# Kernel optimization log

Measured on AMD Instinct MI355X. Metric: run time of the kernel, lower is better.

Reference implementation:

```python
import jax, jax.numpy as jnp
import numpy as np

TOPK = 8            # args.topk
SWAP_RATIO = 0.3    # args.swap_ratio
NUM_SPECIAL = 999   # first non-special wordpiece id in bert-base-uncased


def setup_inputs() -> dict:
    key = jax.random.key(0)
    k0, k1, k2, k3, k4, k5 = jax.random.split(key, 6)
    B, S, V, D = 4, 512, 30522, 768
    return {
        "delta_grad": jax.random.normal(k0, (B, S, D), jnp.float32),
        "src_embeds": jax.random.normal(k1, (B, S, D), jnp.float32),
        "embedding_matrix": jax.random.normal(k2, (V, D), jnp.float32),
        "src_tokens": jax.random.randint(k3, (B, S), 0, V),
        "pred_lm": jax.random.normal(k4, (B, S, V), jnp.float32),
        "attention_mask": jnp.ones((B, S), jnp.int32),
        "rand_u": jax.random.uniform(k5, (B, S), jnp.float32),
    }


def reference(delta_grad, src_embeds, embedding_matrix, src_tokens, pred_lm, attention_mask, rand_u):
    B, S, D = delta_grad.shape
    V = embedding_matrix.shape[0]
    neg_inf = jnp.float32(-np.inf)

    # dir_dot_grad = -(prev_dot - new_dot) = new_dot - prev_dot
    new_dot = jnp.einsum('bsd,vd->bsv', delta_grad, embedding_matrix)   # [B,S,V]
    prev_dot = jnp.einsum('bsd,bsd->bs', delta_grad, src_embeds)        # [B,S]
    dir_dot_grad = new_dot - prev_dot[..., None]

    # pairwise euclidean distance between src_embeds and vocab embeddings
    src_sq = jnp.sum(src_embeds * src_embeds, axis=-1)                  # [B,S]
    vocab_sq = jnp.sum(embedding_matrix * embedding_matrix, axis=-1)    # [V]
    dot = jnp.einsum('bsd,vd->bsv', src_embeds, embedding_matrix)       # [B,S,V]
    sq_norm = src_sq[..., None] + vocab_sq[None, None, :] - 2.0 * dot
    dir_norm = jnp.sqrt(jax.nn.relu(sq_norm) + 1e-20)

    dir_dot_grad = dir_dot_grad / dir_norm

    # LM top-k allowed-token mask (scatter of 0 into a -inf mask in torch)
    _, topk_idx = jax.lax.top_k(pred_lm, TOPK)                          # [B,S,K]
    topk_idx = topk_idx * attention_mask[..., None].astype(topk_idx.dtype)
    bi = jnp.arange(B)[:, None, None]
    si = jnp.arange(S)[None, :, None]
    allowed = jnp.zeros((B, S, V), bool).at[bi, si, topk_idx].set(True)

    filtered = jnp.where(allowed, dir_dot_grad, neg_inf)
    # special tokens [:999] -> -inf (overrides any topk scatter there)
    filtered = jnp.where(jnp.arange(V)[None, None, :] < NUM_SPECIAL, neg_inf, filtered)
    # forbid keeping the original token
    filtered = jnp.where(jnp.arange(V)[None, None, :] == src_tokens[..., None], neg_inf, filtered)

    adv_flip = jnp.argmax(filtered, axis=2)                             # [B,S]

    # swap mask: non-special positions, Bernoulli(swap_ratio)
    no_special = src_tokens >= NUM_SPECIAL
    swap = rand_u > (1.0 - SWAP_RATIO)
    mask_idx = (no_special & swap).astype(src_tokens.dtype)

    adv_tokens = src_tokens * (1 - mask_idx) + adv_flip.astype(src_tokens.dtype) * mask_idx
    return adv_tokens
```

## Files before the change

### kernel.cpp

```cpp
#include <hip/hip_runtime.h>
#include <math.h>

constexpr int TOPK = 8;
constexpr int NUM_SPECIAL = 999;
constexpr int V = 30522;
constexpr int D = 768;
constexpr int BLOCK = 256;
constexpr int V2 = V / 2;
constexpr int NQ = 14;
constexpr int NK = (V2 + BLOCK - 1) / BLOCK;
constexpr int CAP = 512;
constexpr int HOTCAP = 64;

__device__ __forceinline__ unsigned long long fkey(float v, unsigned int idx) {
    unsigned int u = __float_as_uint(v);
    u = ((int)u < 0) ? ~u : (u | 0x80000000u);
    return ((unsigned long long)u << 32) | (unsigned long long)(~idx);
}

__device__ __forceinline__ void net8(float (&L)[TOPK], float t) {
    #pragma unroll
    for (int j = 0; j < TOPK; ++j) {
        float m = fmaxf(L[j], t); t = fminf(L[j], t); L[j] = m;
    }
}

__device__ __forceinline__ void cmpx(float& a, float& b) {
    float m = fmaxf(a, b), n = fminf(a, b); a = m; b = n;
}
__device__ __forceinline__ void bitonic_sort8_desc(float (&v)[TOPK]) {
    cmpx(v[0], v[4]); cmpx(v[1], v[5]); cmpx(v[2], v[6]); cmpx(v[3], v[7]);
    cmpx(v[0], v[2]); cmpx(v[1], v[3]); cmpx(v[4], v[6]); cmpx(v[5], v[7]);
    cmpx(v[0], v[1]); cmpx(v[2], v[3]); cmpx(v[4], v[5]); cmpx(v[6], v[7]);
}

__device__ __forceinline__ void wave_extract8(float (&cur)[TOPK], int lane,
                                              float* dst) {
    #pragma unroll
    for (int r = 0; r < TOPK; ++r) {
        float m = cur[0];
        int ml = lane;
        #pragma unroll
        for (int off = 1; off < 64; off <<= 1) {
            float om = __shfl_xor(m, off, 64);
            int   ol = __shfl_xor(ml, off, 64);
            if (om > m || (om == m && ol < ml)) { m = om; ml = ol; }
        }
        if (lane == ml) {
            #pragma unroll
            for (int j = 0; j < TOPK - 1; ++j) cur[j] = cur[j + 1];
            cur[TOPK - 1] = -INFINITY;
        }
        if (lane == 0) dst[r] = m;
    }
}

__global__ __launch_bounds__(BLOCK, 8) void dvat_kernel(
    const float* __restrict__ delta_grad,
    const float* __restrict__ src_embeds,
    const float* __restrict__ emb,
    const int*   __restrict__ src_tokens,
    const float* __restrict__ pred_lm,
    const int*   __restrict__ attn,
    const float* __restrict__ rand_u,
    int* __restrict__ out)
{
    const int pos = blockIdx.x;
    const int tid = threadIdx.x;
    const int lane = tid & 63;
    const int wave = tid >> 6;

    __shared__ float  sm32[32];
    __shared__ float  s_g8;
    __shared__ int    s_hot[HOTCAP];
    __shared__ int    s_nhot;
    __shared__ int    s_ncand;
    __shared__ unsigned long long sh_cand64[CAP];
    __shared__ int    s_cand[TOPK];
    __shared__ double s_scores[TOPK];
    __shared__ double s_pd[4], s_ssq[4];
    __shared__ float  shf[2 * D];

    if (tid == 0) { s_nhot = 0; s_ncand = 0; }

    const float2* row2 = (const float2*)(pred_lm + (size_t)pos * V);

    float vx[TOPK], vy[TOPK];
    #pragma unroll
    for (int j = 0; j < TOPK; ++j) { vx[j] = -INFINITY; vy[j] = -INFINITY; }

    int i = tid;
    for (int q = 0; q < NQ; ++q, i += 4 * BLOCK) {
        float2 a = row2[i];
        float2 b = row2[i + BLOCK];
        float2 c = row2[i + 2 * BLOCK];
        float2 d = row2[i + 3 * BLOCK];
        net8(vx, a.x); net8(vy, a.y);
        net8(vx, b.x); net8(vy, b.y);
        net8(vx, c.x); net8(vy, c.y);
        net8(vx, d.x); net8(vy, d.y);
    }
    for (; i < V2; i += BLOCK) {
        float2 f = row2[i];
        net8(vx, f.x); net8(vy, f.y);
    }

    float v8[TOPK];
    #pragma unroll
    for (int j = 0; j < TOPK; ++j) v8[j] = fmaxf(vx[j], vy[TOPK - 1 - j]);
    bitonic_sort8_desc(v8);
    const float tmax = v8[0];

    wave_extract8(v8, lane, &sm32[wave * 8]);
    __syncthreads();

    if (wave == 0) {
        float c = (lane < 32) ? sm32[lane] : -INFINITY;
        float m = -INFINITY;
        #pragma unroll
        for (int r = 0; r < TOPK; ++r) {
            m = c; int ml = lane;
            #pragma unroll
            for (int off = 1; off < 64; off <<= 1) {
                float om = __shfl_xor(m, off, 64);
                int   ol = __shfl_xor(ml, off, 64);
                if (om > m || (om == m && ol < ml)) { m = om; ml = ol; }
            }
            if (lane == ml) c = -INFINITY;
        }
        if (lane == 0) s_g8 = m;
    }
    __syncthreads();
    const float g8 = s_g8;

    if (tmax >= g8) {
        int p = atomicAdd(&s_nhot, 1);
        if (p < HOTCAP) s_hot[p] = tid;
    }
    __syncthreads();

    if (s_nhot <= HOTCAP) {
        const int nhot = s_nhot;
        const int total = nhot * NK;
        for (int w = tid; w < total; w += BLOCK) {
            const int h = w / NK;
            const int k = w - h * NK;
            const int i2 = s_hot[h] + (k << 8);
            if (i2 < V2) {
                float2 f = row2[i2];
                if (f.x >= g8) {
                    int p = atomicAdd(&s_ncand, 1);
                    if (p < CAP) sh_cand64[p] = fkey(f.x, (unsigned)(2 * i2));
                }
                if (f.y >= g8) {
                    int p = atomicAdd(&s_ncand, 1);
                    if (p < CAP) sh_cand64[p] = fkey(f.y, (unsigned)(2 * i2 + 1));
                }
            }
        }
    } else {
        for (int i2 = tid; i2 < V2; i2 += BLOCK) {
            float2 f = row2[i2];
            if (f.x >= g8) {
                int p = atomicAdd(&s_ncand, 1);
                if (p < CAP) sh_cand64[p] = fkey(f.x, (unsigned)(2 * i2));
            }
            if (f.y >= g8) {
                int p = atomicAdd(&s_ncand, 1);
                if (p < CAP) sh_cand64[p] = fkey(f.y, (unsigned)(2 * i2 + 1));
            }
        }
    }
    __syncthreads();
    const int ncand = min(s_ncand, CAP);

    for (int it = 0; it < TOPK; ++it) {
        if (tid < 64) {
            unsigned long long m = 0ull; int ms = 0;
            for (int j = tid; j < ncand; j += 64) {
                unsigned long long x = sh_cand64[j];
                if (x > m) { m = x; ms = j; }
            }
            #pragma unroll
            for (int off = 32; off; off >>= 1) {
                unsigned long long om = __shfl_down(m, off, 64);
                int os = __shfl_down(ms, off, 64);
                if (om > m) { m = om; ms = os; }
            }
            if (tid == 0) {
                s_cand[it] = (m == 0ull) ? 0 : (int)(~(unsigned int)m);
                sh_cand64[ms] = 0ull;
            }
        }
        __syncthreads();
    }

    if (tid == 0 && attn[pos] == 0) {
        #pragma unroll
        for (int k = 0; k < TOPK; ++k) s_cand[k] = 0;
    }
    __syncthreads();

    const float* dg = delta_grad + (size_t)pos * D;
    const float* se = src_embeds + (size_t)pos * D;

    double pd = 0.0, ssq = 0.0;
    for (int ii = tid; ii < D; ii += BLOCK) {
        float g = dg[ii], e = se[ii];
        shf[ii] = g;
        shf[D + ii] = e;
        pd  += (double)g * (double)e;
        ssq += (double)e * (double)e;
    }
    #pragma unroll
    for (int off = 32; off; off >>= 1) {
        pd  += __shfl_down(pd, off, 64);
        ssq += __shfl_down(ssq, off, 64);
    }
    if (lane == 0) { s_pd[wave] = pd; s_ssq[wave] = ssq; }
    __syncthreads();

    const double prev_dot = s_pd[0] + s_pd[1] + s_pd[2] + s_pd[3];
    const double src_sq   = s_ssq[0] + s_ssq[1] + s_ssq[2] + s_ssq[3];

    #pragma unroll
    for (int kk = 0; kk < 2; ++kk) {
        const int k = 2 * wave + kk;
        const int v = s_cand[k];
        const float* ev = emb + (size_t)v * D;
        double ddg = 0.0, dse = 0.0, dvv = 0.0;
        for (int ii = lane; ii < D; ii += 64) {
            double e = (double)ev[ii];
            ddg += e * (double)shf[ii];
            dse += e * (double)shf[D + ii];
            dvv += e * e;
        }
        #pragma unroll
        for (int off = 32; off; off >>= 1) {
            ddg += __shfl_down(ddg, off, 64);
            dse += __shfl_down(dse, off, 64);
            dvv += __shfl_down(dvv, off, 64);
        }
        if (lane == 0) {
            double sq = src_sq + dvv - 2.0 * dse;
            if (sq < 0.0) sq = 0.0;
            double dn = sqrt(sq + 1e-20);
            s_scores[k] = (ddg - prev_dot) / dn;
        }
    }
    __syncthreads();

    if (tid == 0) {
        const int src_tok = src_tokens[pos];
        int best = 0;
        double best_s = 0.0;
        bool found = false;
        #pragma unroll
        for (int k = 0; k < TOPK; ++k) {
            const int v = s_cand[k];
            if (v < NUM_SPECIAL || v == src_tok) continue;
            const double sc = s_scores[k];
            if (!found || sc > best_s || (sc == best_s && v < best)) {
                best = v; best_s = sc; found = true;
            }
        }
        const int adv_flip = found ? best : 0;
        const bool no_special = (src_tok >= NUM_SPECIAL);
        const bool swap = (rand_u[pos] > 0.7f);
        out[pos] = (no_special && swap) ? adv_flip : src_tok;
    }
}

extern "C" void kernel_launch(void* const* d_in, const int* in_sizes, int n_in,
                              void* d_out, int out_size, void* d_ws, size_t ws_size,
                              hipStream_t stream) {
    const float* delta_grad = (const float*)d_in[0];
    const float* src_embeds = (const float*)d_in[1];
    const float* emb        = (const float*)d_in[2];
    const int*   src_tokens = (const int*)d_in[3];
    const float* pred_lm    = (const float*)d_in[4];
    const int*   attn       = (const int*)d_in[5];
    const float* randu      = (const float*)d_in[6];
    int* out = (int*)d_out;

    const int BS = in_sizes[3];
    dvat_kernel<<<BS, BLOCK, 0, stream>>>(delta_grad, src_embeds, emb,
                                          src_tokens, pred_lm, attn, randu, out);
}
```

Measured before the change: 414.0 us.

## Use aligned float4 loads with sorted-merge top-8 and hoist per-position dot products

The row scan of pred_lm now uses 16-byte float4 loads aligned by handling a two-element head or tail per row. Each group of 8 values is sorted with a network and merged into the running top-8, which replaces 8 serial insertions. The delta_grad/src_embeds load and reductions move to the start of the kernel, which removes one barrier and overlaps that load with the scan. It adds special-case handling of the edge elements, which is a correctness risk if the alignment arithmetic is wrong.

```diff
diff --git a/kernel.cpp b/kernel.cpp
--- a/kernel.cpp
+++ b/kernel.cpp
@@ -6,9 +6,8 @@
 constexpr int V = 30522;
 constexpr int D = 768;
 constexpr int BLOCK = 256;
-constexpr int V2 = V / 2;
-constexpr int NQ = 14;
-constexpr int NK = (V2 + BLOCK - 1) / BLOCK;
+constexpr int NF4 = 7630;
+constexpr int NK4 = 30;
 constexpr int CAP = 512;
 constexpr int HOTCAP = 64;
 
@@ -18,20 +17,35 @@
     return ((unsigned long long)u << 32) | (unsigned long long)(~idx);
 }
 
+__device__ __forceinline__ void cmpx(float& a, float& b) {
+    float m = fmaxf(a, b), n = fminf(a, b); a = m; b = n;
+}
+
+__device__ __forceinline__ void sort8_desc(float (&c)[8]) {
+    cmpx(c[0],c[1]); cmpx(c[2],c[3]); cmpx(c[4],c[5]); cmpx(c[6],c[7]);
+    cmpx(c[0],c[2]); cmpx(c[1],c[3]); cmpx(c[1],c[2]);
+    cmpx(c[4],c[6]); cmpx(c[5],c[7]); cmpx(c[5],c[6]);
+    cmpx(c[0],c[4]); cmpx(c[1],c[5]); cmpx(c[2],c[6]); cmpx(c[3],c[7]);
+    cmpx(c[2],c[4]); cmpx(c[3],c[5]);
+    cmpx(c[1],c[2]); cmpx(c[3],c[4]); cmpx(c[5],c[6]);
+}
+
+__device__ __forceinline__ void merge_top8(float (&R)[8], const float (&C)[8]) {
+    float m[8];
+    #pragma unroll
+    for (int j = 0; j < 8; ++j) m[j] = fmaxf(R[j], C[7 - j]);
+    cmpx(m[0],m[4]); cmpx(m[1],m[5]); cmpx(m[2],m[6]); cmpx(m[3],m[7]);
+    cmpx(m[0],m[2]); cmpx(m[1],m[3]); cmpx(m[4],m[6]); cmpx(m[5],m[7]);
+    cmpx(m[0],m[1]); cmpx(m[2],m[3]); cmpx(m[4],m[5]); cmpx(m[6],m[7]);
+    #pragma unroll
+    for (int j = 0; j < 8; ++j) R[j] = m[j];
+}
+
 __device__ __forceinline__ void net8(float (&L)[TOPK], float t) {
     #pragma unroll
     for (int j = 0; j < TOPK; ++j) {
         float m = fmaxf(L[j], t); t = fminf(L[j], t); L[j] = m;
     }
-}
-
-__device__ __forceinline__ void cmpx(float& a, float& b) {
-    float m = fmaxf(a, b), n = fminf(a, b); a = m; b = n;
-}
-__device__ __forceinline__ void bitonic_sort8_desc(float (&v)[TOPK]) {
-    cmpx(v[0], v[4]); cmpx(v[1], v[5]); cmpx(v[2], v[6]); cmpx(v[3], v[7]);
-    cmpx(v[0], v[2]); cmpx(v[1], v[3]); cmpx(v[4], v[6]); cmpx(v[5], v[7]);
-    cmpx(v[0], v[1]); cmpx(v[2], v[3]); cmpx(v[4], v[5]); cmpx(v[6], v[7]);
 }
 
 __device__ __forceinline__ void wave_extract8(float (&cur)[TOPK], int lane,
@@ -83,35 +97,61 @@
 
     if (tid == 0) { s_nhot = 0; s_ncand = 0; }
 
-    const float2* row2 = (const float2*)(pred_lm + (size_t)pos * V);
-
-    float vx[TOPK], vy[TOPK];
-    #pragma unroll
-    for (int j = 0; j < TOPK; ++j) { vx[j] = -INFINITY; vy[j] = -INFINITY; }
-
-    int i = tid;
-    for (int q = 0; q < NQ; ++q, i += 4 * BLOCK) {
-        float2 a = row2[i];
-        float2 b = row2[i + BLOCK];
-        float2 c = row2[i + 2 * BLOCK];
-        float2 d = row2[i + 3 * BLOCK];
-        net8(vx, a.x); net8(vy, a.y);
-        net8(vx, b.x); net8(vy, b.y);
-        net8(vx, c.x); net8(vy, c.y);
-        net8(vx, d.x); net8(vy, d.y);
-    }
-    for (; i < V2; i += BLOCK) {
-        float2 f = row2[i];
-        net8(vx, f.x); net8(vy, f.y);
-    }
-
-    float v8[TOPK];
-    #pragma unroll
-    for (int j = 0; j < TOPK; ++j) v8[j] = fmaxf(vx[j], vy[TOPK - 1 - j]);
-    bitonic_sort8_desc(v8);
-    const float tmax = v8[0];
-
-    wave_extract8(v8, lane, &sm32[wave * 8]);
+    {
+        const float* dg = delta_grad + (size_t)pos * D;
+        const float* se = src_embeds + (size_t)pos * D;
+        double pd = 0.0, ssq = 0.0;
+        if (tid < D / 4) {
+            float4 g = ((const float4*)dg)[tid];
+            float4 e = ((const float4*)se)[tid];
+            ((float4*)shf)[tid] = g;
+            ((float4*)(shf + D))[tid] = e;
+            pd  = (double)g.x * e.x + (double)g.y * e.y
+                + (double)g.z * e.z + (double)g.w * e.w;
+            ssq = (double)e.x * e.x + (double)e.y * e.y
+                + (double)e.z * e.z + (double)e.w * e.w;
+        }
+        #pragma unroll
+        for (int off = 32; off; off >>= 1) {
+            pd  += __shfl_down(pd, off, 64);
+            ssq += __shfl_down(ssq, off, 64);
+        }
+        if (lane == 0) { s_pd[wave] = pd; s_ssq[wave] = ssq; }
+    }
+
+    const float* row = pred_lm + (size_t)pos * V;
+    const int al = (pos & 1) ? 2 : 0;
+    const float4* f4 = (const float4*)(row + al);
+
+    float R[8];
+    #pragma unroll
+    for (int j = 0; j < 8; ++j) R[j] = -INFINITY;
+
+    int ia = tid;
+    for (int p = 0; p < 7; ++p, ia += 4 * BLOCK) {
+        float4 a = f4[ia];
+        float4 b = f4[ia + BLOCK];
+        float4 c = f4[ia + 2 * BLOCK];
+        float4 d = f4[ia + 3 * BLOCK];
+        float ca[8] = {a.x, a.y, a.z, a.w, b.x, b.y, b.z, b.w};
+        sort8_desc(ca); merge_top8(R, ca);
+        float cb[8] = {c.x, c.y, c.z, c.w, d.x, d.y, d.z, d.w};
+        sort8_desc(cb); merge_top8(R, cb);
+    }
+    {
+        float4 a = f4[ia];
+        float4 b = {-INFINITY, -INFINITY, -INFINITY, -INFINITY};
+        if (ia + BLOCK < NF4) b = f4[ia + BLOCK];
+        float ca[8] = {a.x, a.y, a.z, a.w, b.x, b.y, b.z, b.w};
+        sort8_desc(ca); merge_top8(R, ca);
+    }
+    if (tid == 0) {
+        if (al) { net8(R, row[0]);     net8(R, row[1]); }
+        else    { net8(R, row[V - 2]); net8(R, row[V - 1]); }
+    }
+    const float tmax = R[0];
+
+    wave_extract8(R, lane, &sm32[wave * 8]);
     __syncthreads();
 
     if (wave == 0) {
@@ -137,38 +177,41 @@
         int p = atomicAdd(&s_nhot, 1);
         if (p < HOTCAP) s_hot[p] = tid;
     }
+    if (tid == 0) {
+        if (al) {
+            if (row[0] >= g8) { int p = atomicAdd(&s_ncand, 1); if (p < CAP) sh_cand64[p] = fkey(row[0], 0u); }
+            if (row[1] >= g8) { int p = atomicAdd(&s_ncand, 1); if (p < CAP) sh_cand64[p] = fkey(row[1], 1u); }
+        } else {
+            if (row[V-2] >= g8) { int p = atomicAdd(&s_ncand, 1); if (p < CAP) sh_cand64[p] = fkey(row[V-2], (unsigned)(V-2)); }
+            if (row[V-1] >= g8) { int p = atomicAdd(&s_ncand, 1); if (p < CAP) sh_cand64[p] = fkey(row[V-1], (unsigned)(V-1)); }
+        }
+    }
     __syncthreads();
 
     if (s_nhot <= HOTCAP) {
         const int nhot = s_nhot;
-        const int total = nhot * NK;
+        const int total = nhot * NK4;
         for (int w = tid; w < total; w += BLOCK) {
-            const int h = w / NK;
-            const int k = w - h * NK;
-            const int i2 = s_hot[h] + (k << 8);
-            if (i2 < V2) {
-                float2 f = row2[i2];
-                if (f.x >= g8) {
-                    int p = atomicAdd(&s_ncand, 1);
-                    if (p < CAP) sh_cand64[p] = fkey(f.x, (unsigned)(2 * i2));
-                }
-                if (f.y >= g8) {
-                    int p = atomicAdd(&s_ncand, 1);
-                    if (p < CAP) sh_cand64[p] = fkey(f.y, (unsigned)(2 * i2 + 1));
-                }
+            const int h = w / NK4;
+            const int k = w - h * NK4;
+            const int i4 = s_hot[h] + (k << 8);
+            if (i4 < NF4) {
+                float4 f = f4[i4];
+                const unsigned base = (unsigned)(al + 4 * i4);
+                if (f.x >= g8) { int p = atomicAdd(&s_ncand, 1); if (p < CAP) sh_cand64[p] = fkey(f.x, base); }
+                if (f.y >= g8) { int p = atomicAdd(&s_ncand, 1); if (p < CAP) sh_cand64[p] = fkey(f.y, base + 1); }
+                if (f.z >= g8) { int p = atomicAdd(&s_ncand, 1); if (p < CAP) sh_cand64[p] = fkey(f.z, base + 2); }
+                if (f.w >= g8) { int p = atomicAdd(&s_ncand, 1); if (p < CAP) sh_cand64[p] = fkey(f.w, base + 3); }
             }
         }
     } else {
-        for (int i2 = tid; i2 < V2; i2 += BLOCK) {
-            float2 f = row2[i2];
-            if (f.x >= g8) {
-                int p = atomicAdd(&s_ncand, 1);
-                if (p < CAP) sh_cand64[p] = fkey(f.x, (unsigned)(2 * i2));
-            }
-            if (f.y >= g8) {
-                int p = atomicAdd(&s_ncand, 1);
-                if (p < CAP) sh_cand64[p] = fkey(f.y, (unsigned)(2 * i2 + 1));
-            }
+        for (int i4 = tid; i4 < NF4; i4 += BLOCK) {
+            float4 f = f4[i4];
+            const unsigned base = (unsigned)(al + 4 * i4);
+            if (f.x >= g8) { int p = atomicAdd(&s_ncand, 1); if (p < CAP) sh_cand64[p] = fkey(f.x, base); }
+            if (f.y >= g8) { int p = atomicAdd(&s_ncand, 1); if (p < CAP) sh_cand64[p] = fkey(f.y, base + 1); }
+            if (f.z >= g8) { int p = atomicAdd(&s_ncand, 1); if (p < CAP) sh_cand64[p] = fkey(f.z, base + 2); }
+            if (f.w >= g8) { int p = atomicAdd(&s_ncand, 1); if (p < CAP) sh_cand64[p] = fkey(f.w, base + 3); }
         }
     }
     __syncthreads();
@@ -199,25 +242,6 @@
         #pragma unroll
         for (int k = 0; k < TOPK; ++k) s_cand[k] = 0;
     }
-    __syncthreads();
-
-    const float* dg = delta_grad + (size_t)pos * D;
-    const float* se = src_embeds + (size_t)pos * D;
-
-    double pd = 0.0, ssq = 0.0;
-    for (int ii = tid; ii < D; ii += BLOCK) {
-        float g = dg[ii], e = se[ii];
-        shf[ii] = g;
-        shf[D + ii] = e;
-        pd  += (double)g * (double)e;
-        ssq += (double)e * (double)e;
-    }
-    #pragma unroll
-    for (int off = 32; off; off >>= 1) {
-        pd  += __shfl_down(pd, off, 64);
-        ssq += __shfl_down(ssq, off, 64);
-    }
-    if (lane == 0) { s_pd[wave] = pd; s_ssq[wave] = ssq; }
     __syncthreads();
 
     const double prev_dot = s_pd[0] + s_pd[1] + s_pd[2] + s_pd[3];
```

New measurement: 421.4 us. Within noise of the previous version (+1.8%).
